# Kernel optimization log

Measured on AMD Instinct MI355X. Metric: run time of the kernel, lower is better.

Reference implementation:

```python
import jax, jax.numpy as jnp
import numpy as np

B, S, D, H, R = 4, 2048, 4096, 4096, 16
Q_SCALE = K_SCALE = V_SCALE = 1.0


def setup_inputs() -> dict:
    key = jax.random.key(0)
    ks = jax.random.split(key, 10)
    sd = 0.02
    return {
        "x": jax.random.normal(ks[0], (B, S, D), dtype=jnp.float32),
        "q_weight": jax.random.normal(ks[1], (H, D), dtype=jnp.float32) * sd,
        "k_weight": jax.random.normal(ks[2], (H, D), dtype=jnp.float32) * sd,
        "v_weight": jax.random.normal(ks[3], (H, D), dtype=jnp.float32) * sd,
        "q_A": jax.random.normal(ks[4], (R, D), dtype=jnp.float32) * sd,
        "q_B": jax.random.normal(ks[5], (H, R), dtype=jnp.float32) * sd,
        "k_A": jax.random.normal(ks[6], (R, D), dtype=jnp.float32) * sd,
        "k_B": jax.random.normal(ks[7], (H, R), dtype=jnp.float32) * sd,
        "v_A": jax.random.normal(ks[8], (R, D), dtype=jnp.float32) * sd,
        "v_B": jax.random.normal(ks[9], (H, R), dtype=jnp.float32) * sd,
    }


def _matmul_lora(x, W, A, Bm, s):
    # x: [B,S,D]; W: [H,D] (torch Linear layout, applied as x @ W.T)
    # LoRA: A [R,D], B [H,R] -> out += (x @ A.T) @ (s * B.T)
    main = jnp.einsum("bsd,hd->bsh", x, W)
    lora = jnp.einsum("bsr,hr->bsh", jnp.einsum("bsd,rd->bsr", x, A), s * Bm)
    return main + lora


def reference(x, q_weight, k_weight, v_weight, q_A, q_B, k_A, k_B, v_A, v_B):
    Q = _matmul_lora(x, q_weight, q_A, q_B, Q_SCALE)
    K = _matmul_lora(x, k_weight, k_A, k_B, K_SCALE)
    V = _matmul_lora(x, v_weight, v_A, v_B, V_SCALE)
    return (Q, K, V)
```

## Files before the change

kernel.cpp:

```cpp
#include <hip/hip_runtime.h>


typedef __bf16 bf16x8 __attribute__((ext_vector_type(8)));
typedef float f32x4 __attribute__((ext_vector_type(4)));

#define GLL16(g, l)                                                        \
  __builtin_amdgcn_global_load_lds(                                        \
      (const __attribute__((address_space(1))) unsigned int*)(g),          \
      (__attribute__((address_space(3))) unsigned int*)(l), 16, 0, 0)

#define BAR()                                                              \
  {                                                                        \
    __builtin_amdgcn_sched_barrier(0);                                     \
    __builtin_amdgcn_s_barrier();                                          \
  }
#define WLG(n) asm volatile("s_waitcnt lgkmcnt(" #n ")" ::: "memory")
#define WVM(n) asm volatile("s_waitcnt vmcnt(" #n ")" ::: "memory")

#define LDV(p) (*reinterpret_cast<const bf16x8*>(p))

#define RDA(dst, base, M0)                                                 \
  _Pragma("unroll") for (int mm = 0; mm < 4; ++mm) {                       \
    dst[0][mm] = LDV((base) + ((M0) + mm) * 1024 + swk0);                  \
    dst[1][mm] = LDV((base) + ((M0) + mm) * 1024 + swk1);                  \
  }
#define RDB(dst, base, N0)                                                 \
  _Pragma("unroll") for (int nn = 0; nn < 2; ++nn) {                       \
    dst[0][nn] = LDV((base) + ((N0) + nn) * 1024 + swk0);                  \
    dst[1][nn] = LDV((base) + ((N0) + nn) * 1024 + swk1);                  \
  }

#define MFQ(AQ, BQ, MB, NB)                                                \
  {                                                                        \
    __builtin_amdgcn_s_setprio(1);                                         \
    _Pragma("unroll") for (int ks = 0; ks < 2; ++ks)                       \
        _Pragma("unroll") for (int mm = 0; mm < 4; ++mm)                   \
            _Pragma("unroll") for (int nn = 0; nn < 2; ++nn)               \
                acc[(MB) + mm][(NB) + nn] =                                \
                    __builtin_amdgcn_mfma_f32_16x16x32_bf16(               \
                        AQ[ks][mm], BQ[ks][nn], acc[(MB) + mm][(NB) + nn], \
                        0, 0, 0);                                          \
    __builtin_amdgcn_s_setprio(0);                                         \
  }

#define STG_A(db, h, ko)                                                   \
  {                                                                        \
    GLL16(sa + (size_t)((h)*128) * 4096 + (ko),                            \
          (char*)smem + (db)*65536 + (h)*16384 + tid * 16);                \
    GLL16(sa + (size_t)((h)*128 + 64) * 4096 + (ko),                       \
          (char*)smem + (db)*65536 + (h)*16384 + 8192 + tid * 16);         \
  }
#define STG_B(db, h, ko)                                                   \
  {                                                                        \
    GLL16(sb + (size_t)((h)*128) * 4096 + (ko),                            \
          (char*)smem + (db)*65536 + 32768 + (h)*16384 + tid * 16);        \
    GLL16(sb + (size_t)((h)*128 + 64) * 4096 + (ko),                       \
          (char*)smem + (db)*65536 + 32768 + (h)*16384 + 8192 + tid * 16); \
  }

__device__ __forceinline__ unsigned int f2b(float f) {
  unsigned int u = __builtin_bit_cast(unsigned int, f);
  u += 0x7FFFu + ((u >> 16) & 1u);
  return u >> 16;
}

__global__ void cvt_x_kernel(const float* __restrict__ x,
                             unsigned short* __restrict__ xb, long n8) {
  long i = (long)blockIdx.x * blockDim.x + threadIdx.x;
  if (i >= n8) return;
  const float4* xp = reinterpret_cast<const float4*>(x) + 2 * i;
  float4 v0 = xp[0];
  float4 v1 = xp[1];
  uint4 o;
  o.x = f2b(v0.x) | (f2b(v0.y) << 16);
  o.y = f2b(v0.z) | (f2b(v0.w) << 16);
  o.z = f2b(v1.x) | (f2b(v1.y) << 16);
  o.w = f2b(v1.z) | (f2b(v1.w) << 16);
  reinterpret_cast<uint4*>(xb)[i] = o;
}

__global__ void fold_w_kernel(const float* __restrict__ W,
                              const float* __restrict__ Amat,
                              const float* __restrict__ Bmat,
                              unsigned short* __restrict__ Wb) {
  int gi = blockIdx.x * 256 + threadIdx.x;
  int d0 = (gi & 511) * 8;
  int h = gi >> 9;
  const float4* wp = reinterpret_cast<const float4*>(W + (size_t)h * 4096 + d0);
  float4 w0 = wp[0], w1 = wp[1];
  float acc[8] = {w0.x, w0.y, w0.z, w0.w, w1.x, w1.y, w1.z, w1.w};
  const float* bh = Bmat + h * 16;
#pragma unroll
  for (int r = 0; r < 16; ++r) {
    float bv = bh[r];
    const float4* ap =
        reinterpret_cast<const float4*>(Amat + (size_t)r * 4096 + d0);
    float4 a0 = ap[0], a1 = ap[1];
    acc[0] += bv * a0.x; acc[1] += bv * a0.y;
    acc[2] += bv * a0.z; acc[3] += bv * a0.w;
    acc[4] += bv * a1.x; acc[5] += bv * a1.y;
    acc[6] += bv * a1.z; acc[7] += bv * a1.w;
  }
  uint4 o;
  o.x = f2b(acc[0]) | (f2b(acc[1]) << 16);
  o.y = f2b(acc[2]) | (f2b(acc[3]) << 16);
  o.z = f2b(acc[4]) | (f2b(acc[5]) << 16);
  o.w = f2b(acc[6]) | (f2b(acc[7]) << 16);
  reinterpret_cast<uint4*>(Wb)[gi] = o;
}

__global__ __launch_bounds__(512, 2) void gemm_kernel(
    const unsigned short* __restrict__ Xb,
    const unsigned short* __restrict__ Wb, float* __restrict__ out) {
  __shared__ unsigned short smem[65536];

  const int tid = threadIdx.x;
  const int lane = tid & 63;
  const int wid = tid >> 6;
  const int wm = wid >> 2;
  const int wn = wid & 3;

  int bid = blockIdx.x;
  int swz = (bid & 7) * 192 + (bid >> 3);
  int p = swz >> 9;
  int r = swz & 511;
  int brow = r >> 4;
  int bcol = r & 15;

  const unsigned short* GA = Xb + (size_t)brow * 256 * 4096;
  const unsigned short* GB =
      Wb + (size_t)p * 16777216UL + (size_t)bcol * 256 * 4096;

  const int srow = tid >> 3;
  const int sslot = (tid & 7) ^ (srow & 7);
  const unsigned short* sa = GA + (size_t)srow * 4096 + sslot * 8;
  const unsigned short* sb = GB + (size_t)srow * 4096 + sslot * 8;

  const int lrow = lane & 15;
  const int g = lane >> 4;
  const int swk0 = (g ^ (lane & 7)) * 8;
  const int swk1 = ((4 + g) ^ (lane & 7)) * 8;
  const __bf16* sm = (const __bf16*)smem;
  const __bf16* arA0 = sm + wm * 8192 + lrow * 64;
  const __bf16* arB0 = sm + 16384 + (wn >> 1) * 8192 + ((wn & 1) * 64 + lrow) * 64;
  const __bf16* arA1 = arA0 + 32768;
  const __bf16* arB1 = arB0 + 32768;

  f32x4 acc[8][4];
#pragma unroll
  for (int m = 0; m < 8; ++m)
#pragma unroll
    for (int n = 0; n < 4; ++n) acc[m][n] = {0.f, 0.f, 0.f, 0.f};

  STG_B(0, 0, 0); STG_B(0, 1, 0); STG_A(0, 0, 0); STG_A(0, 1, 0);
  WVM(4);
  STG_B(1, 0, 64); STG_B(1, 1, 64); STG_A(1, 0, 64);
  WVM(6);
  BAR();

  bf16x8 aLo[2][4], aHi[2][4], bLo[2][2], bHi[2][2];

  for (int i = 0; i < 32; ++i) {
    const bool st = (i < 31);
    const size_t koD1 = (size_t)(2 * i + 1) * 64;
    const size_t koN0 = (size_t)(2 * i + 2) * 64;
    const size_t koN1 = (size_t)(2 * i + 3) * 64;

    RDA(aLo, arA0, 0);
    RDB(bLo, arB0, 0);
    STG_A(1, 1, koD1);
    WLG(8);
    BAR();
    WLG(0);
    MFQ(aLo, bLo, 0, 0);
    BAR();
    RDB(bHi, arB0, 2);
    if (st) STG_B(0, 0, koN0);
    BAR();
    WLG(0);
    MFQ(aLo, bHi, 0, 2);
    BAR();
    RDA(aHi, arA0, 4);
    if (st) STG_B(0, 1, koN0);
    BAR();
    WLG(0);
    MFQ(aHi, bHi, 4, 2);
    BAR();
    if (st) {
      STG_A(0, 0, koN0);
      WVM(6);
    } else {
      WVM(0);
    }
    BAR();
    MFQ(aHi, bLo, 4, 0);
    BAR();

    RDA(aLo, arA1, 0);
    RDB(bLo, arB1, 0);
    if (st) STG_A(0, 1, koN0);
    WLG(8);
    BAR();
    WLG(0);
    MFQ(aLo, bLo, 0, 0);
    BAR();
    RDB(bHi, arB1, 2);
    if (st) STG_B(1, 0, koN1);
    BAR();
    WLG(0);
    MFQ(aLo, bHi, 0, 2);
    BAR();
    RDA(aHi, arA1, 4);
    if (st) STG_B(1, 1, koN1);
    BAR();
    WLG(0);
    MFQ(aHi, bHi, 4, 2);
    BAR();
    if (st) {
      STG_A(1, 0, koN1);
      WVM(6);
    }
    BAR();
    MFQ(aHi, bLo, 4, 0);
    BAR();
  }

  float* Cp = out + (size_t)p * 33554432UL +
              ((size_t)(brow * 256 + wm * 128 + g * 4)) * 4096 +
              (bcol * 256 + wn * 64 + lrow);
#pragma unroll
  for (int m = 0; m < 8; ++m)
#pragma unroll
    for (int q = 0; q < 4; ++q) {
      float* rp = Cp + (size_t)(m * 16 + q) * 4096;
#pragma unroll
      for (int n = 0; n < 4; ++n) rp[n * 16] = acc[m][n][q];
    }
}

extern "C" void kernel_launch(void* const* d_in, const int* in_sizes, int n_in,
                              void* d_out, int out_size, void* d_ws,
                              size_t ws_size, hipStream_t stream) {
  const float* x = (const float*)d_in[0];
  const float* wq = (const float*)d_in[1];
  const float* wk = (const float*)d_in[2];
  const float* wv = (const float*)d_in[3];
  const float* qa = (const float*)d_in[4];
  const float* qb = (const float*)d_in[5];
  const float* ka = (const float*)d_in[6];
  const float* kb = (const float*)d_in[7];
  const float* va = (const float*)d_in[8];
  const float* vb = (const float*)d_in[9];

  unsigned short* xb = (unsigned short*)d_ws;
  unsigned short* wb = xb + 8192UL * 4096UL;

  cvt_x_kernel<<<16384, 256, 0, stream>>>(x, xb, 8192L * 4096 / 8);
  fold_w_kernel<<<8192, 256, 0, stream>>>(wq, qa, qb, wb);
  fold_w_kernel<<<8192, 256, 0, stream>>>(wk, ka, kb, wb + 16777216UL);
  fold_w_kernel<<<8192, 256, 0, stream>>>(wv, va, vb, wb + 33554432UL);
  gemm_kernel<<<1536, 512, 0, stream>>>(xb, wb, (float*)d_out);
}
```

Baseline: 914.5 us.

## Switch GEMM to 32x32x16 MFMA tiles and merge prep kernels into one launch

The GEMM inner loop now uses 32x32x16 bf16 MFMA instructions with 16-float accumulators instead of 16x16x32, and the LDS fragment reads and swizzle offsets are reorganised to match the larger tile. The goal is fewer MFMA issues and fewer LDS reads per unit of work. Separately, the x-conversion kernel and the three weight-folding kernels become one prep kernel that branches on block index, removing three launches. The risks are extra register pressure from the larger fragments and a new epilogue write pattern that may coalesce differently.

```diff
diff --git a/kernel.cpp b/kernel.cpp
--- a/kernel.cpp
+++ b/kernel.cpp
@@ -2,7 +2,7 @@
 
 
 typedef __bf16 bf16x8 __attribute__((ext_vector_type(8)));
-typedef float f32x4 __attribute__((ext_vector_type(4)));
+typedef float f32x16 __attribute__((ext_vector_type(16)));
 
 #define GLL16(g, l)                                                        \
   __builtin_amdgcn_global_load_lds(                                        \
@@ -19,27 +19,29 @@
 
 #define LDV(p) (*reinterpret_cast<const bf16x8*>(p))
 
-#define RDA(dst, base, M0)                                                 \
-  _Pragma("unroll") for (int mm = 0; mm < 4; ++mm) {                       \
-    dst[0][mm] = LDV((base) + ((M0) + mm) * 1024 + swk0);                  \
-    dst[1][mm] = LDV((base) + ((M0) + mm) * 1024 + swk1);                  \
-  }
-#define RDB(dst, base, N0)                                                 \
-  _Pragma("unroll") for (int nn = 0; nn < 2; ++nn) {                       \
-    dst[0][nn] = LDV((base) + ((N0) + nn) * 1024 + swk0);                  \
-    dst[1][nn] = LDV((base) + ((N0) + nn) * 1024 + swk1);                  \
-  }
-
-#define MFQ(AQ, BQ, MB, NB)                                                \
+#define RDA2(dst, base, M0)                                                \
+  _Pragma("unroll") for (int mm = 0; mm < 2; ++mm) {                       \
+    dst[mm][0] = LDV((base) + ((M0) + mm) * 2048 + swk0);                  \
+    dst[mm][1] = LDV((base) + ((M0) + mm) * 2048 + swk1);                  \
+    dst[mm][2] = LDV((base) + ((M0) + mm) * 2048 + swk2);                  \
+    dst[mm][3] = LDV((base) + ((M0) + mm) * 2048 + swk3);                  \
+  }
+#define RDB4(dst, base, NT)                                                \
+  {                                                                        \
+    dst[0] = LDV((base) + (NT)*2048 + swk0);                               \
+    dst[1] = LDV((base) + (NT)*2048 + swk1);                               \
+    dst[2] = LDV((base) + (NT)*2048 + swk2);                               \
+    dst[3] = LDV((base) + (NT)*2048 + swk3);                               \
+  }
+
+#define MFQ(AQ, BQ, MP, NT)                                                \
   {                                                                        \
     __builtin_amdgcn_s_setprio(1);                                         \
-    _Pragma("unroll") for (int ks = 0; ks < 2; ++ks)                       \
-        _Pragma("unroll") for (int mm = 0; mm < 4; ++mm)                   \
-            _Pragma("unroll") for (int nn = 0; nn < 2; ++nn)               \
-                acc[(MB) + mm][(NB) + nn] =                                \
-                    __builtin_amdgcn_mfma_f32_16x16x32_bf16(               \
-                        AQ[ks][mm], BQ[ks][nn], acc[(MB) + mm][(NB) + nn], \
-                        0, 0, 0);                                          \
+    _Pragma("unroll") for (int ks = 0; ks < 4; ++ks)                       \
+        _Pragma("unroll") for (int mm = 0; mm < 2; ++mm)                   \
+            acc[(MP)*2 + mm][NT] =                                         \
+                __builtin_amdgcn_mfma_f32_32x32x16_bf16(                   \
+                    AQ[mm][ks], BQ[ks], acc[(MP)*2 + mm][NT], 0, 0, 0);    \
     __builtin_amdgcn_s_setprio(0);                                         \
   }
 
@@ -64,49 +66,67 @@
   return u >> 16;
 }
 
-__global__ void cvt_x_kernel(const float* __restrict__ x,
-                             unsigned short* __restrict__ xb, long n8) {
-  long i = (long)blockIdx.x * blockDim.x + threadIdx.x;
-  if (i >= n8) return;
-  const float4* xp = reinterpret_cast<const float4*>(x) + 2 * i;
-  float4 v0 = xp[0];
-  float4 v1 = xp[1];
-  uint4 o;
-  o.x = f2b(v0.x) | (f2b(v0.y) << 16);
-  o.y = f2b(v0.z) | (f2b(v0.w) << 16);
-  o.z = f2b(v1.x) | (f2b(v1.y) << 16);
-  o.w = f2b(v1.z) | (f2b(v1.w) << 16);
-  reinterpret_cast<uint4*>(xb)[i] = o;
-}
-
-__global__ void fold_w_kernel(const float* __restrict__ W,
-                              const float* __restrict__ Amat,
-                              const float* __restrict__ Bmat,
-                              unsigned short* __restrict__ Wb) {
-  int gi = blockIdx.x * 256 + threadIdx.x;
-  int d0 = (gi & 511) * 8;
-  int h = gi >> 9;
-  const float4* wp = reinterpret_cast<const float4*>(W + (size_t)h * 4096 + d0);
-  float4 w0 = wp[0], w1 = wp[1];
-  float acc[8] = {w0.x, w0.y, w0.z, w0.w, w1.x, w1.y, w1.z, w1.w};
-  const float* bh = Bmat + h * 16;
-#pragma unroll
-  for (int r = 0; r < 16; ++r) {
-    float bv = bh[r];
-    const float4* ap =
-        reinterpret_cast<const float4*>(Amat + (size_t)r * 4096 + d0);
-    float4 a0 = ap[0], a1 = ap[1];
-    acc[0] += bv * a0.x; acc[1] += bv * a0.y;
-    acc[2] += bv * a0.z; acc[3] += bv * a0.w;
-    acc[4] += bv * a1.x; acc[5] += bv * a1.y;
-    acc[6] += bv * a1.z; acc[7] += bv * a1.w;
-  }
-  uint4 o;
-  o.x = f2b(acc[0]) | (f2b(acc[1]) << 16);
-  o.y = f2b(acc[2]) | (f2b(acc[3]) << 16);
-  o.z = f2b(acc[4]) | (f2b(acc[5]) << 16);
-  o.w = f2b(acc[6]) | (f2b(acc[7]) << 16);
-  reinterpret_cast<uint4*>(Wb)[gi] = o;
+__global__ void prep_kernel(const float* __restrict__ x,
+                            const float* __restrict__ w0,
+                            const float* __restrict__ w1,
+                            const float* __restrict__ w2,
+                            const float* __restrict__ a0,
+                            const float* __restrict__ b0,
+                            const float* __restrict__ a1,
+                            const float* __restrict__ b1,
+                            const float* __restrict__ a2,
+                            const float* __restrict__ b2,
+                            unsigned short* __restrict__ xb,
+                            unsigned short* __restrict__ wb) {
+  const int bid = blockIdx.x;
+  const int tid = threadIdx.x;
+  if (bid < 8192) {
+    long base = ((long)bid * 256 + tid) * 2;
+    const float4* xp = reinterpret_cast<const float4*>(x) + base * 2;
+#pragma unroll
+    for (int j = 0; j < 2; ++j) {
+      float4 v0 = xp[2 * j];
+      float4 v1 = xp[2 * j + 1];
+      uint4 o;
+      o.x = f2b(v0.x) | (f2b(v0.y) << 16);
+      o.y = f2b(v0.z) | (f2b(v0.w) << 16);
+      o.z = f2b(v1.x) | (f2b(v1.y) << 16);
+      o.w = f2b(v1.z) | (f2b(v1.w) << 16);
+      reinterpret_cast<uint4*>(xb)[base + j] = o;
+    }
+  } else {
+    const int fb = bid - 8192;
+    const int proj = fb >> 13;
+    const float* W = (proj == 0) ? w0 : ((proj == 1) ? w1 : w2);
+    const float* Amat = (proj == 0) ? a0 : ((proj == 1) ? a1 : a2);
+    const float* Bmat = (proj == 0) ? b0 : ((proj == 1) ? b1 : b2);
+    unsigned short* Wo = wb + (size_t)proj * 16777216UL;
+    int gi = (fb & 8191) * 256 + tid;
+    int d0 = (gi & 511) * 8;
+    int h = gi >> 9;
+    const float4* wp =
+        reinterpret_cast<const float4*>(W + (size_t)h * 4096 + d0);
+    float4 w0v = wp[0], w1v = wp[1];
+    float acc[8] = {w0v.x, w0v.y, w0v.z, w0v.w, w1v.x, w1v.y, w1v.z, w1v.w};
+    const float* bh = Bmat + h * 16;
+#pragma unroll
+    for (int r = 0; r < 16; ++r) {
+      float bv = bh[r];
+      const float4* ap =
+          reinterpret_cast<const float4*>(Amat + (size_t)r * 4096 + d0);
+      float4 A0 = ap[0], A1 = ap[1];
+      acc[0] += bv * A0.x; acc[1] += bv * A0.y;
+      acc[2] += bv * A0.z; acc[3] += bv * A0.w;
+      acc[4] += bv * A1.x; acc[5] += bv * A1.y;
+      acc[6] += bv * A1.z; acc[7] += bv * A1.w;
+    }
+    uint4 o;
+    o.x = f2b(acc[0]) | (f2b(acc[1]) << 16);
+    o.y = f2b(acc[2]) | (f2b(acc[3]) << 16);
+    o.z = f2b(acc[4]) | (f2b(acc[5]) << 16);
+    o.w = f2b(acc[6]) | (f2b(acc[7]) << 16);
+    reinterpret_cast<uint4*>(Wo)[gi] = o;
+  }
 }
 
 __global__ __launch_bounds__(512, 2) void gemm_kernel(
@@ -136,21 +156,27 @@
   const unsigned short* sa = GA + (size_t)srow * 4096 + sslot * 8;
   const unsigned short* sb = GB + (size_t)srow * 4096 + sslot * 8;
 
-  const int lrow = lane & 15;
-  const int g = lane >> 4;
-  const int swk0 = (g ^ (lane & 7)) * 8;
-  const int swk1 = ((4 + g) ^ (lane & 7)) * 8;
+  const int l31 = lane & 31;
+  const int h2 = lane >> 5;
+  const int bx = lane & 7;
+  const int swk0 = (((0 * 2 + h2) ^ bx)) * 8;
+  const int swk1 = (((1 * 2 + h2) ^ bx)) * 8;
+  const int swk2 = (((2 * 2 + h2) ^ bx)) * 8;
+  const int swk3 = (((3 * 2 + h2) ^ bx)) * 8;
   const __bf16* sm = (const __bf16*)smem;
-  const __bf16* arA0 = sm + wm * 8192 + lrow * 64;
-  const __bf16* arB0 = sm + 16384 + (wn >> 1) * 8192 + ((wn & 1) * 64 + lrow) * 64;
+  const __bf16* arA0 = sm + wm * 8192 + l31 * 64;
+  const __bf16* arB0 =
+      sm + 16384 + (wn >> 1) * 8192 + ((wn & 1) * 64 + l31) * 64;
   const __bf16* arA1 = arA0 + 32768;
   const __bf16* arB1 = arB0 + 32768;
 
-  f32x4 acc[8][4];
-#pragma unroll
-  for (int m = 0; m < 8; ++m)
-#pragma unroll
-    for (int n = 0; n < 4; ++n) acc[m][n] = {0.f, 0.f, 0.f, 0.f};
+  f32x16 acc[4][2];
+#pragma unroll
+  for (int m = 0; m < 4; ++m)
+#pragma unroll
+    for (int n = 0; n < 2; ++n)
+#pragma unroll
+      for (int e = 0; e < 16; ++e) acc[m][n][e] = 0.f;
 
   STG_B(0, 0, 0); STG_B(0, 1, 0); STG_A(0, 0, 0); STG_A(0, 1, 0);
   WVM(4);
@@ -158,7 +184,7 @@
   WVM(6);
   BAR();
 
-  bf16x8 aLo[2][4], aHi[2][4], bLo[2][2], bHi[2][2];
+  bf16x8 aLo[2][4], aHi[2][4], bLo[4], bHi[4];
 
   for (int i = 0; i < 32; ++i) {
     const bool st = (i < 31);
@@ -166,25 +192,25 @@
     const size_t koN0 = (size_t)(2 * i + 2) * 64;
     const size_t koN1 = (size_t)(2 * i + 3) * 64;
 
-    RDA(aLo, arA0, 0);
-    RDB(bLo, arB0, 0);
+    RDA2(aLo, arA0, 0);
+    RDB4(bLo, arB0, 0);
     STG_A(1, 1, koD1);
     WLG(8);
     BAR();
     WLG(0);
     MFQ(aLo, bLo, 0, 0);
     BAR();
-    RDB(bHi, arB0, 2);
+    RDB4(bHi, arB0, 1);
     if (st) STG_B(0, 0, koN0);
     BAR();
     WLG(0);
-    MFQ(aLo, bHi, 0, 2);
-    BAR();
-    RDA(aHi, arA0, 4);
+    MFQ(aLo, bHi, 0, 1);
+    BAR();
+    RDA2(aHi, arA0, 2);
     if (st) STG_B(0, 1, koN0);
     BAR();
     WLG(0);
-    MFQ(aHi, bHi, 4, 2);
+    MFQ(aHi, bHi, 1, 1);
     BAR();
     if (st) {
       STG_A(0, 0, koN0);
@@ -193,48 +219,51 @@
       WVM(0);
     }
     BAR();
-    MFQ(aHi, bLo, 4, 0);
-    BAR();
-
-    RDA(aLo, arA1, 0);
-    RDB(bLo, arB1, 0);
+    MFQ(aHi, bLo, 1, 0);
+    BAR();
+
+    RDA2(aLo, arA1, 0);
+    RDB4(bLo, arB1, 0);
     if (st) STG_A(0, 1, koN0);
     WLG(8);
     BAR();
     WLG(0);
     MFQ(aLo, bLo, 0, 0);
     BAR();
-    RDB(bHi, arB1, 2);
+    RDB4(bHi, arB1, 1);
     if (st) STG_B(1, 0, koN1);
     BAR();
     WLG(0);
-    MFQ(aLo, bHi, 0, 2);
-    BAR();
-    RDA(aHi, arA1, 4);
+    MFQ(aLo, bHi, 0, 1);
+    BAR();
+    RDA2(aHi, arA1, 2);
     if (st) STG_B(1, 1, koN1);
     BAR();
     WLG(0);
-    MFQ(aHi, bHi, 4, 2);
+    MFQ(aHi, bHi, 1, 1);
     BAR();
     if (st) {
       STG_A(1, 0, koN1);
       WVM(6);
     }
     BAR();
-    MFQ(aHi, bLo, 4, 0);
+    MFQ(aHi, bLo, 1, 0);
     BAR();
   }
 
   float* Cp = out + (size_t)p * 33554432UL +
-              ((size_t)(brow * 256 + wm * 128 + g * 4)) * 4096 +
-              (bcol * 256 + wn * 64 + lrow);
-#pragma unroll
-  for (int m = 0; m < 8; ++m)
-#pragma unroll
-    for (int q = 0; q < 4; ++q) {
-      float* rp = Cp + (size_t)(m * 16 + q) * 4096;
-#pragma unroll
-      for (int n = 0; n < 4; ++n) rp[n * 16] = acc[m][n][q];
+              ((size_t)(brow * 256 + wm * 128 + 4 * h2)) * 4096 +
+              (bcol * 256 + wn * 64 + l31);
+#pragma unroll
+  for (int mt = 0; mt < 4; ++mt)
+#pragma unroll
+    for (int nt = 0; nt < 2; ++nt) {
+      const f32x16 v = acc[mt][nt];
+#pragma unroll
+      for (int reg = 0; reg < 16; ++reg) {
+        const int row = mt * 32 + (reg & 3) + 8 * (reg >> 2);
+        Cp[(size_t)row * 4096 + nt * 32] = v[reg];
+      }
     }
 }
 
@@ -255,9 +284,7 @@
   unsigned short* xb = (unsigned short*)d_ws;
   unsigned short* wb = xb + 8192UL * 4096UL;
 
-  cvt_x_kernel<<<16384, 256, 0, stream>>>(x, xb, 8192L * 4096 / 8);
-  fold_w_kernel<<<8192, 256, 0, stream>>>(wq, qa, qb, wb);
-  fold_w_kernel<<<8192, 256, 0, stream>>>(wk, ka, kb, wb + 16777216UL);
-  fold_w_kernel<<<8192, 256, 0, stream>>>(wv, va, vb, wb + 33554432UL);
+  prep_kernel<<<32768, 256, 0, stream>>>(x, wq, wk, wv, qa, qb, ka, kb, va,
+                                         vb, xb, wb);
   gemm_kernel<<<1536, 512, 0, stream>>>(xb, wb, (float*)d_out);
 }
```

Result: slower. 998.4 us (+9.2%).
